# Optimization experiments

Hardware: AMD Instinct MI355X
Metric: run time of the kernel (lower is better)

Reference implementation:

```python
import jax, jax.numpy as jnp
import numpy as np

V, D, H, B, M, T, PAD = 32000, 512, 3, 32, 512, 4, 1


def setup_inputs() -> dict:
    key = jax.random.key(0)
    ks = jax.random.split(key, 10)
    def emb_tables(k):
        t = 0.1 * jax.random.normal(k, (H + 1, V, D), jnp.float32)
        return t.at[:, PAD, :].set(0.0)  # padding_idx rows are zero
    C_enc = emb_tables(ks[0])
    C_dec = emb_tables(ks[1])
    gru_w_ih = 0.1 * jax.random.normal(ks[2], (3 * D, D), jnp.float32)
    gru_w_hh = 0.1 * jax.random.normal(ks[3], (3 * D, D), jnp.float32)
    gru_b_ih = jnp.zeros((3 * D,), jnp.float32)
    gru_b_hh = jnp.zeros((3 * D,), jnp.float32)
    W1_w = 0.1 * jax.random.normal(ks[4], (V, 2 * D), jnp.float32)
    W1_b = jnp.zeros((V,), jnp.float32)
    story = jax.random.randint(ks[5], (B, M, T), 0, V, jnp.int32)
    enc_query = jax.random.randint(ks[6], (B,), 0, V, jnp.int32)
    return {"story": story, "enc_query": enc_query, "C_enc": C_enc,
            "C_dec": C_dec, "gru_w_ih": gru_w_ih, "gru_w_hh": gru_w_hh,
            "gru_b_ih": gru_b_ih, "gru_b_hh": gru_b_hh, "W1_w": W1_w,
            "W1_b": W1_b}


def _mem_embed(table, story):
    # table [V, D], story [B, M, T] -> sum-pooled memory [B, M, D]
    return jnp.sum(table[story], axis=2)


def _forward(C_enc, C_dec, gru_w_ih, gru_w_hh, gru_b_ih, gru_b_hh,
             W1_w, W1_b, story, enc_query):
    # ---- EncoderMemNN.forward (eval mode, no unk_mask dropout) ----
    u = jnp.zeros((story.shape[0], D), C_enc.dtype)
    for hop in range(H):
        m_A = _mem_embed(C_enc[hop], story)            # [B, M, D]
        prob = jax.nn.softmax(jnp.einsum('bmd,bd->bm', m_A, u), axis=1)
        m_C = _mem_embed(C_enc[hop + 1], story)        # [B, M, D]
        u = u + jnp.einsum('bmd,bm->bd', m_C, prob)
    enc_hidden = u                                     # decoder_hidden[0]

    # ---- DecoderrMemNN.ptrMemDecoder: single GRU step ----
    x = C_dec[0][enc_query]                            # [B, D]
    gi = x @ gru_w_ih.T + gru_b_ih                     # [B, 3D]
    gh = enc_hidden @ gru_w_hh.T + gru_b_hh            # [B, 3D]
    i_r, i_z, i_n = jnp.split(gi, 3, axis=1)
    h_r, h_z, h_n = jnp.split(gh, 3, axis=1)
    r = jax.nn.sigmoid(i_r + h_r)
    z = jax.nn.sigmoid(i_z + h_z)
    n = jnp.tanh(i_n + r * h_n)
    hidden = (1.0 - z) * n + z * enc_hidden            # new GRU hidden [B, D]

    # ---- DecoderrMemNN.load_memory: m_story[h] = sum-pooled C_dec[h] ----
    m_story = [_mem_embed(C_dec[h], story) for h in range(H + 1)]

    # ---- multi-hop pointer attention ----
    u0 = hidden
    uk = hidden
    p_vocab = None
    for hop in range(H):
        prob_lg = jnp.einsum('bmd,bd->bm', m_story[hop], uk)   # [B, M]
        prob = jax.nn.softmax(prob_lg, axis=1)
        o_k = jnp.einsum('bmd,bm->bd', m_story[hop + 1], prob)  # [B, D]
        if hop == 0:
            p_vocab = jnp.concatenate([u0, o_k], axis=1) @ W1_w.T + W1_b
        uk = uk + o_k
    p_ptr = prob_lg                                    # logits from last hop
    return p_ptr, p_vocab, hidden[None]                # hidden [1, B, D]


def reference(story, enc_query, C_enc, C_dec, gru_w_ih, gru_w_hh,
              gru_b_ih, gru_b_hh, W1_w, W1_b):
    return _forward(C_enc, C_dec, gru_w_ih, gru_w_hh, gru_b_ih, gru_b_hh,
                    W1_w, W1_b, story, enc_query)
```

## Files before the change

kernel.cpp:

```cpp
#include <hip/hip_runtime.h>
#include <math.h>

#define DD 512
#define MM 512
#define BB 32
#define TT 4
#define VV 32000

__global__ __launch_bounds__(256) void poolwsum_kernel(const float* __restrict__ table,
                                                       const int* __restrict__ story,
                                                       const float* __restrict__ s,
                                                       float* __restrict__ partial) {
  __shared__ float wrow[64];
  __shared__ int rows[64];
  __shared__ float red[16];
  __shared__ float4 comb[128];
  int b = blockIdx.x >> 5;
  int c = blockIdx.x & 31;
  int t = threadIdx.x;
  if (s) {
    float v0 = s[b * MM + t], v1 = s[b * MM + t + 256];
    float mx = fmaxf(v0, v1);
#pragma unroll
    for (int off = 32; off > 0; off >>= 1) mx = fmaxf(mx, __shfl_xor(mx, off));
    if ((t & 63) == 0) red[t >> 6] = mx;
    __syncthreads();
    mx = fmaxf(fmaxf(red[0], red[1]), fmaxf(red[2], red[3]));
    float e0 = expf(v0 - mx), e1 = expf(v1 - mx);
    float sm = e0 + e1;
#pragma unroll
    for (int off = 32; off > 0; off >>= 1) sm += __shfl_xor(sm, off);
    if ((t & 63) == 0) red[8 + (t >> 6)] = sm;
    __syncthreads();
    sm = red[8] + red[9] + red[10] + red[11];
    float inv = 1.0f / sm;
    if (t < 64) {
      rows[t] = story[((b << 9) + (c << 4)) * TT + t];
      wrow[t] = expf(s[b * MM + (c << 4) + (t >> 2)] - mx) * inv;
    }
  } else {
    if (t < 64) {
      rows[t] = story[((b << 9) + (c << 4)) * TT + t];
      wrow[t] = 1.0f / MM;
    }
  }
  __syncthreads();
  int half = t >> 7;
  int col = t & 127;
  float4 acc = make_float4(0.f, 0.f, 0.f, 0.f);
  for (int i = half; i < 64; i += 2) {
    float wm = wrow[i];
    float4 v = *((const float4*)(table + (size_t)rows[i] * DD) + col);
    acc.x += wm * v.x; acc.y += wm * v.y;
    acc.z += wm * v.z; acc.w += wm * v.w;
  }
  if (half) comb[col] = acc;
  __syncthreads();
  if (!half) {
    float4 o = comb[col];
    acc.x += o.x; acc.y += o.y; acc.z += o.z; acc.w += o.w;
    ((float4*)(partial + (size_t)blockIdx.x * DD))[col] = acc;
  }
}

__global__ void wsumB_kernel(const float* __restrict__ partial,
                             const float* __restrict__ prev,
                             float* __restrict__ uout) {
  int i = blockIdx.x * 256 + threadIdx.x;
  int b = i >> 9, d = i & 511;
  float acc = prev ? prev[i] : 0.f;
  const float* pp = partial + (size_t)b * 32 * DD + d;
#pragma unroll
  for (int c = 0; c < 32; ++c) acc += pp[c * DD];
  uout[i] = acc;
}

__global__ void wsumB2_kernel(const float* __restrict__ partial,
                              const float* __restrict__ hid,
                              float* __restrict__ uk, float* __restrict__ hc) {
  int i = blockIdx.x * 256 + threadIdx.x;
  int b = i >> 9, d = i & 511;
  float ov = 0.f;
  const float* pp = partial + (size_t)b * 32 * DD + d;
#pragma unroll
  for (int c = 0; c < 32; ++c) ov += pp[c * DD];
  float hv = hid[i];
  uk[i] = hv + ov;
  hc[b * 1024 + d] = hv;
  hc[b * 1024 + 512 + d] = ov;
}

__global__ __launch_bounds__(256) void pooldot_kernel(const float* __restrict__ table,
                                                      const int* __restrict__ story,
                                                      const float* __restrict__ u,
                                                      float* __restrict__ s) {
  int wave = (blockIdx.x << 2) + (threadIdx.x >> 6);
  int lane = threadIdx.x & 63;
  int b = wave >> 9;
  const int* st = story + wave * TT;
  size_t r0 = (size_t)st[0] * DD, r1 = (size_t)st[1] * DD;
  size_t r2 = (size_t)st[2] * DD, r3 = (size_t)st[3] * DD;
  const float4* t4 = (const float4*)table;
  const float4* ur = (const float4*)(u + (size_t)b * DD);
  float acc = 0.f;
#pragma unroll
  for (int h = 0; h < 2; ++h) {
    int c = (h << 6) + lane;
    float4 a = t4[(r0 >> 2) + c];
    float4 bb = t4[(r1 >> 2) + c];
    float4 cc = t4[(r2 >> 2) + c];
    float4 d = t4[(r3 >> 2) + c];
    float4 q = ur[c];
    acc += (a.x + bb.x + cc.x + d.x) * q.x;
    acc += (a.y + bb.y + cc.y + d.y) * q.y;
    acc += (a.z + bb.z + cc.z + d.z) * q.z;
    acc += (a.w + bb.w + cc.w + d.w) * q.w;
  }
#pragma unroll
  for (int off = 32; off > 0; off >>= 1) acc += __shfl_xor(acc, off);
  if (lane == 0) s[wave] = acc;
}

__global__ __launch_bounds__(256) void matvec_kernel(const float* __restrict__ W,
                                                     const float* __restrict__ bias,
                                                     const float* __restrict__ vin,
                                                     const int* __restrict__ q,
                                                     const float* __restrict__ table,
                                                     float* __restrict__ out) {
  int idx = (blockIdx.x << 2) + (threadIdx.x >> 6);
  int lane = threadIdx.x & 63;
  int b = idx / 1536;
  int j = idx - b * 1536;
  const float* xb = vin ? (vin + (size_t)b * DD) : (table + (size_t)q[b] * DD);
  const float4* Wr = (const float4*)(W + (size_t)j * DD);
  const float4* xr = (const float4*)xb;
  float acc = 0.f;
#pragma unroll
  for (int h = 0; h < 2; ++h) {
    int c = (h << 6) + lane;
    float4 a = Wr[c];
    float4 qv = xr[c];
    acc += a.x * qv.x + a.y * qv.y + a.z * qv.z + a.w * qv.w;
  }
#pragma unroll
  for (int off = 32; off > 0; off >>= 1) acc += __shfl_xor(acc, off);
  if (lane == 0) out[idx] = acc + bias[j];
}

__global__ void gate_kernel(const float* __restrict__ gi, const float* __restrict__ gh,
                            const float* __restrict__ u, float* __restrict__ hidden,
                            float* __restrict__ out_h) {
  int i = blockIdx.x * 256 + threadIdx.x;
  int b = i >> 9, d = i & 511;
  const float* gib = gi + b * 1536;
  const float* ghb = gh + b * 1536;
  float i_r = gib[d], i_z = gib[d + 512], i_n = gib[d + 1024];
  float h_r = ghb[d], h_z = ghb[d + 512], h_n = ghb[d + 1024];
  float r = 1.f / (1.f + expf(-(i_r + h_r)));
  float z = 1.f / (1.f + expf(-(i_z + h_z)));
  float n = tanhf(i_n + r * h_n);
  float h = (1.f - z) * n + z * u[i];
  hidden[i] = h;
  out_h[i] = h;
}

__global__ __launch_bounds__(256) void pvocab_kernel(const float* __restrict__ Hcat,
                                                     const float* __restrict__ W1,
                                                     float* __restrict__ partc) {
  __shared__ float As[32][36];
  __shared__ float Bs[32][68];
  int t = threadIdx.x;
  int vt = blockIdx.x >> 1;
  int kh = blockIdx.x & 1;
  int v0 = vt * 64;
  int kbase = kh << 9;
  int tb = t >> 5;
  int tv = t & 31;
  int br = t >> 2;
  int bk = (t & 3) << 3;
  const float* Wp = W1 + (size_t)(v0 + br) * 1024 + kbase + bk;
  int ab = t >> 3;
  int ak = (t & 7) << 2;
  const float* Ap = Hcat + (size_t)ab * 1024 + kbase + ak;

  float acc[4][2] = {{0.f, 0.f}, {0.f, 0.f}, {0.f, 0.f}, {0.f, 0.f}};

  float4 aReg = *(const float4*)(Ap);
  float4 wReg0 = *(const float4*)(Wp);
  float4 wReg1 = *(const float4*)(Wp + 4);

  for (int k0 = 0; k0 < 512; k0 += 32) {
    As[ak + 0][ab] = aReg.x; As[ak + 1][ab] = aReg.y;
    As[ak + 2][ab] = aReg.z; As[ak + 3][ab] = aReg.w;
    Bs[bk + 0][br] = wReg0.x; Bs[bk + 1][br] = wReg0.y;
    Bs[bk + 2][br] = wReg0.z; Bs[bk + 3][br] = wReg0.w;
    Bs[bk + 4][br] = wReg1.x; Bs[bk + 5][br] = wReg1.y;
    Bs[bk + 6][br] = wReg1.z; Bs[bk + 7][br] = wReg1.w;
    __syncthreads();
    if (k0 + 32 < 512) {
      aReg = *(const float4*)(Ap + k0 + 32);
      wReg0 = *(const float4*)(Wp + k0 + 32);
      wReg1 = *(const float4*)(Wp + k0 + 36);
    }
#pragma unroll
    for (int k = 0; k < 32; ++k) {
      float2 bv = *(const float2*)&Bs[k][tv * 2];
      float4 av = *(const float4*)&As[k][tb * 4];
      acc[0][0] += av.x * bv.x; acc[0][1] += av.x * bv.y;
      acc[1][0] += av.y * bv.x; acc[1][1] += av.y * bv.y;
      acc[2][0] += av.z * bv.x; acc[2][1] += av.z * bv.y;
      acc[3][0] += av.w * bv.x; acc[3][1] += av.w * bv.y;
    }
    __syncthreads();
  }
  int v = v0 + tv * 2;
  float* base = partc + (size_t)kh * 32 * VV;
#pragma unroll
  for (int i = 0; i < 4; ++i) {
    float2 r;
    r.x = acc[i][0];
    r.y = acc[i][1];
    *(float2*)(base + (size_t)(tb * 4 + i) * VV + v) = r;
  }
}

__global__ void pvreduce_kernel(const float* __restrict__ partc,
                                const float* __restrict__ W1b,
                                float* __restrict__ out) {
  int v = blockIdx.x * 256 + threadIdx.x;
  int b = blockIdx.y;
  size_t o = (size_t)b * VV + v;
  out[o] = partc[o] + partc[(size_t)32 * VV + o] + W1b[v];
}

extern "C" void kernel_launch(void* const* d_in, const int* in_sizes, int n_in,
                              void* d_out, int out_size, void* d_ws, size_t ws_size,
                              hipStream_t stream) {
  const int* story = (const int*)d_in[0];
  const int* q = (const int*)d_in[1];
  const float* C_enc = (const float*)d_in[2];
  const float* C_dec = (const float*)d_in[3];
  const float* W_ih = (const float*)d_in[4];
  const float* W_hh = (const float*)d_in[5];
  const float* b_ih = (const float*)d_in[6];
  const float* b_hh = (const float*)d_in[7];
  const float* W1 = (const float*)d_in[8];
  const float* W1b = (const float*)d_in[9];
  float* out = (float*)d_out;

  const size_t VD = (size_t)VV * DD;
  const float* C1 = C_enc + 1 * VD;
  const float* C2 = C_enc + 2 * VD;
  const float* C3 = C_enc + 3 * VD;
  const float* D0 = C_dec + 0 * VD;
  const float* D1 = C_dec + 1 * VD;
  const float* D2 = C_dec + 2 * VD;

  float* part = (float*)d_ws;
  float* partc = part + (size_t)BB * 32 * DD;
  float* u = partc + (size_t)2 * BB * VV;
  float* s = u + BB * DD;
  float* gi = s + BB * MM;
  float* gh = gi + BB * 3 * DD;
  float* hid = gh + BB * 3 * DD;
  float* uk = hid + BB * DD;
  float* hc = uk + BB * DD;

  float* p_ptr_out = out;
  float* p_vocab_out = out + BB * MM;
  float* hid_out = out + BB * MM + (size_t)BB * VV;

  dim3 blk(256);
  const int pwGrid = BB * 32;
  const int pdGrid = BB * MM / 4;
  const int mvGrid = BB * 3 * DD / 4;
  const int ewGrid = BB * DD / 256;

  poolwsum_kernel<<<pwGrid, blk, 0, stream>>>(C1, story, nullptr, part);
  wsumB_kernel<<<ewGrid, blk, 0, stream>>>(part, nullptr, u);
  pooldot_kernel<<<pdGrid, blk, 0, stream>>>(C1, story, u, s);
  poolwsum_kernel<<<pwGrid, blk, 0, stream>>>(C2, story, s, part);
  wsumB_kernel<<<ewGrid, blk, 0, stream>>>(part, u, u);
  pooldot_kernel<<<pdGrid, blk, 0, stream>>>(C2, story, u, s);
  poolwsum_kernel<<<pwGrid, blk, 0, stream>>>(C3, story, s, part);
  wsumB_kernel<<<ewGrid, blk, 0, stream>>>(part, u, u);

  matvec_kernel<<<mvGrid, blk, 0, stream>>>(W_ih, b_ih, nullptr, q, C_dec, gi);
  matvec_kernel<<<mvGrid, blk, 0, stream>>>(W_hh, b_hh, u, nullptr, nullptr, gh);
  gate_kernel<<<ewGrid, blk, 0, stream>>>(gi, gh, u, hid, hid_out);

  pooldot_kernel<<<pdGrid, blk, 0, stream>>>(D0, story, hid, s);
  poolwsum_kernel<<<pwGrid, blk, 0, stream>>>(D1, story, s, part);
  wsumB2_kernel<<<ewGrid, blk, 0, stream>>>(part, hid, uk, hc);
  pooldot_kernel<<<pdGrid, blk, 0, stream>>>(D1, story, uk, s);
  poolwsum_kernel<<<pwGrid, blk, 0, stream>>>(D2, story, s, part);
  wsumB_kernel<<<ewGrid, blk, 0, stream>>>(part, uk, uk);
  pooldot_kernel<<<pdGrid, blk, 0, stream>>>(D2, story, uk, p_ptr_out);

  pvocab_kernel<<<VV / 64 * 2, blk, 0, stream>>>(hc, W1, partc);
  pvreduce_kernel<<<dim3(125, 32), blk, 0, stream>>>(partc, W1b, p_vocab_out);
}
```

Measured before the change: 302.7 us.

## Replace gathered pooled dot with dense vocab GEMM plus index gather

Each pooled-memory dot product now scores every vocabulary row against u as a split-K GEMM (u times the table transposed). A light kernel then sums the precomputed scores at the four story indices per memory slot. The goal is to swap about 65K random 2KB row gathers per hop for one streaming read of the table. The cost is extra GEMM arithmetic and partial-score buffers written and re-read. The p_vocab GEMM also moves from 2-way to 4-way split-K, which doubles the block count but also the reduction traffic.

Result: slower. 373.5 us (+23.4%).

```diff
diff --git a/kernel.cpp b/kernel.cpp
--- a/kernel.cpp
+++ b/kernel.cpp
@@ -6,6 +6,7 @@
 #define BB 32
 #define TT 4
 #define VV 32000
+#define BV ((size_t)BB * VV)
 
 __global__ __launch_bounds__(256) void poolwsum_kernel(const float* __restrict__ table,
                                                        const int* __restrict__ story,
@@ -90,35 +91,79 @@
   hc[b * 1024 + 512 + d] = ov;
 }
 
-__global__ __launch_bounds__(256) void pooldot_kernel(const float* __restrict__ table,
-                                                      const int* __restrict__ story,
-                                                      const float* __restrict__ u,
-                                                      float* __restrict__ s) {
-  int wave = (blockIdx.x << 2) + (threadIdx.x >> 6);
-  int lane = threadIdx.x & 63;
-  int b = wave >> 9;
-  const int* st = story + wave * TT;
-  size_t r0 = (size_t)st[0] * DD, r1 = (size_t)st[1] * DD;
-  size_t r2 = (size_t)st[2] * DD, r3 = (size_t)st[3] * DD;
-  const float4* t4 = (const float4*)table;
-  const float4* ur = (const float4*)(u + (size_t)b * DD);
+__global__ __launch_bounds__(256) void dotV_kernel(const float* __restrict__ u,
+                                                   const float* __restrict__ C,
+                                                   float* __restrict__ part) {
+  __shared__ float As[32][36];
+  __shared__ float Bs[32][68];
+  int t = threadIdx.x;
+  int vt = blockIdx.x >> 2;
+  int kh = blockIdx.x & 3;
+  int v0 = vt * 64;
+  int kbase = kh << 7;
+  int tb = t >> 5;
+  int tv = t & 31;
+  int br = t >> 2;
+  int bk = (t & 3) << 3;
+  const float* Wp = C + (size_t)(v0 + br) * DD + kbase + bk;
+  int ab = t >> 3;
+  int ak = (t & 7) << 2;
+  const float* Ap = u + (size_t)ab * DD + kbase + ak;
+
+  float acc[4][2] = {{0.f, 0.f}, {0.f, 0.f}, {0.f, 0.f}, {0.f, 0.f}};
+
+  float4 aReg = *(const float4*)(Ap);
+  float4 wReg0 = *(const float4*)(Wp);
+  float4 wReg1 = *(const float4*)(Wp + 4);
+
+  for (int k0 = 0; k0 < 128; k0 += 32) {
+    As[ak + 0][ab] = aReg.x; As[ak + 1][ab] = aReg.y;
+    As[ak + 2][ab] = aReg.z; As[ak + 3][ab] = aReg.w;
+    Bs[bk + 0][br] = wReg0.x; Bs[bk + 1][br] = wReg0.y;
+    Bs[bk + 2][br] = wReg0.z; Bs[bk + 3][br] = wReg0.w;
+    Bs[bk + 4][br] = wReg1.x; Bs[bk + 5][br] = wReg1.y;
+    Bs[bk + 6][br] = wReg1.z; Bs[bk + 7][br] = wReg1.w;
+    __syncthreads();
+    if (k0 + 32 < 128) {
+      aReg = *(const float4*)(Ap + k0 + 32);
+      wReg0 = *(const float4*)(Wp + k0 + 32);
+      wReg1 = *(const float4*)(Wp + k0 + 36);
+    }
+#pragma unroll
+    for (int k = 0; k < 32; ++k) {
+      float2 bv = *(const float2*)&Bs[k][tv * 2];
+      float4 av = *(const float4*)&As[k][tb * 4];
+      acc[0][0] += av.x * bv.x; acc[0][1] += av.x * bv.y;
+      acc[1][0] += av.y * bv.x; acc[1][1] += av.y * bv.y;
+      acc[2][0] += av.z * bv.x; acc[2][1] += av.z * bv.y;
+      acc[3][0] += av.w * bv.x; acc[3][1] += av.w * bv.y;
+    }
+    __syncthreads();
+  }
+  int v = v0 + tv * 2;
+  float* base = part + (size_t)kh * BV;
+#pragma unroll
+  for (int i = 0; i < 4; ++i) {
+    float2 r;
+    r.x = acc[i][0];
+    r.y = acc[i][1];
+    *(float2*)(base + (size_t)(tb * 4 + i) * VV + v) = r;
+  }
+}
+
+__global__ void gatherS_kernel(const float* __restrict__ part,
+                               const int* __restrict__ story,
+                               float* __restrict__ outv) {
+  int i = blockIdx.x * 256 + threadIdx.x;
+  int b = i >> 9;
+  int4 ix = *(const int4*)(story + (size_t)i * 4);
   float acc = 0.f;
 #pragma unroll
-  for (int h = 0; h < 2; ++h) {
-    int c = (h << 6) + lane;
-    float4 a = t4[(r0 >> 2) + c];
-    float4 bb = t4[(r1 >> 2) + c];
-    float4 cc = t4[(r2 >> 2) + c];
-    float4 d = t4[(r3 >> 2) + c];
-    float4 q = ur[c];
-    acc += (a.x + bb.x + cc.x + d.x) * q.x;
-    acc += (a.y + bb.y + cc.y + d.y) * q.y;
-    acc += (a.z + bb.z + cc.z + d.z) * q.z;
-    acc += (a.w + bb.w + cc.w + d.w) * q.w;
-  }
-#pragma unroll
-  for (int off = 32; off > 0; off >>= 1) acc += __shfl_xor(acc, off);
-  if (lane == 0) s[wave] = acc;
+  for (int kh = 0; kh < 4; ++kh) {
+    const float* dv = part + (size_t)kh * BV + (size_t)b * VV;
+    acc += dv[ix.x] + dv[ix.y] + dv[ix.z] + dv[ix.w];
+  }
+  outv[i] = acc;
 }
 
 __global__ __launch_bounds__(256) void matvec_kernel(const float* __restrict__ W,
@@ -170,10 +215,10 @@
   __shared__ float As[32][36];
   __shared__ float Bs[32][68];
   int t = threadIdx.x;
-  int vt = blockIdx.x >> 1;
-  int kh = blockIdx.x & 1;
+  int vt = blockIdx.x >> 2;
+  int kh = blockIdx.x & 3;
   int v0 = vt * 64;
-  int kbase = kh << 9;
+  int kbase = kh << 8;
   int tb = t >> 5;
   int tv = t & 31;
   int br = t >> 2;
@@ -189,7 +234,7 @@
   float4 wReg0 = *(const float4*)(Wp);
   float4 wReg1 = *(const float4*)(Wp + 4);
 
-  for (int k0 = 0; k0 < 512; k0 += 32) {
+  for (int k0 = 0; k0 < 256; k0 += 32) {
     As[ak + 0][ab] = aReg.x; As[ak + 1][ab] = aReg.y;
     As[ak + 2][ab] = aReg.z; As[ak + 3][ab] = aReg.w;
     Bs[bk + 0][br] = wReg0.x; Bs[bk + 1][br] = wReg0.y;
@@ -197,7 +242,7 @@
     Bs[bk + 4][br] = wReg1.x; Bs[bk + 5][br] = wReg1.y;
     Bs[bk + 6][br] = wReg1.z; Bs[bk + 7][br] = wReg1.w;
     __syncthreads();
-    if (k0 + 32 < 512) {
+    if (k0 + 32 < 256) {
       aReg = *(const float4*)(Ap + k0 + 32);
       wReg0 = *(const float4*)(Wp + k0 + 32);
       wReg1 = *(const float4*)(Wp + k0 + 36);
@@ -214,7 +259,7 @@
     __syncthreads();
   }
   int v = v0 + tv * 2;
-  float* base = partc + (size_t)kh * 32 * VV;
+  float* base = partc + (size_t)kh * BV;
 #pragma unroll
   for (int i = 0; i < 4; ++i) {
     float2 r;
@@ -230,7 +275,7 @@
   int v = blockIdx.x * 256 + threadIdx.x;
   int b = blockIdx.y;
   size_t o = (size_t)b * VV + v;
-  out[o] = partc[o] + partc[(size_t)32 * VV + o] + W1b[v];
+  out[o] = partc[o] + partc[BV + o] + partc[2 * BV + o] + partc[3 * BV + o] + W1b[v];
 }
 
 extern "C" void kernel_launch(void* const* d_in, const int* in_sizes, int n_in,
@@ -258,7 +303,8 @@
 
   float* part = (float*)d_ws;
   float* partc = part + (size_t)BB * 32 * DD;
-  float* u = partc + (size_t)2 * BB * VV;
+  float* dvp = partc + 4 * BV;
+  float* u = dvp + 4 * BV;
   float* s = u + BB * DD;
   float* gi = s + BB * MM;
   float* gh = gi + BB * 3 * DD;
@@ -272,16 +318,18 @@
 
   dim3 blk(256);
   const int pwGrid = BB * 32;
-  const int pdGrid = BB * MM / 4;
+  const int dvGrid = VV / 64 * 4;
   const int mvGrid = BB * 3 * DD / 4;
   const int ewGrid = BB * DD / 256;
 
   poolwsum_kernel<<<pwGrid, blk, 0, stream>>>(C1, story, nullptr, part);
   wsumB_kernel<<<ewGrid, blk, 0, stream>>>(part, nullptr, u);
-  pooldot_kernel<<<pdGrid, blk, 0, stream>>>(C1, story, u, s);
+  dotV_kernel<<<dvGrid, blk, 0, stream>>>(u, C1, dvp);
+  gatherS_kernel<<<ewGrid, blk, 0, stream>>>(dvp, story, s);
   poolwsum_kernel<<<pwGrid, blk, 0, stream>>>(C2, story, s, part);
   wsumB_kernel<<<ewGrid, blk, 0, stream>>>(part, u, u);
-  pooldot_kernel<<<pdGrid, blk, 0, stream>>>(C2, story, u, s);
+  dotV_kernel<<<dvGrid, blk, 0, stream>>>(u, C2, dvp);
+  gatherS_kernel<<<ewGrid, blk, 0, stream>>>(dvp, story, s);
   poolwsum_kernel<<<pwGrid, blk, 0, stream>>>(C3, story, s, part);
   wsumB_kernel<<<ewGrid, blk, 0, stream>>>(part, u, u);
 
@@ -289,14 +337,17 @@
   matvec_kernel<<<mvGrid, blk, 0, stream>>>(W_hh, b_hh, u, nullptr, nullptr, gh);
   gate_kernel<<<ewGrid, blk, 0, stream>>>(gi, gh, u, hid, hid_out);
 
-  pooldot_kernel<<<pdGrid, blk, 0, stream>>>(D0, story, hid, s);
+  dotV_kernel<<<dvGrid, blk, 0, stream>>>(hid, D0, dvp);
+  gatherS_kernel<<<ewGrid, blk, 0, stream>>>(dvp, story, s);
   poolwsum_kernel<<<pwGrid, blk, 0, stream>>>(D1, story, s, part);
   wsumB2_kernel<<<ewGrid, blk, 0, stream>>>(part, hid, uk, hc);
-  pooldot_kernel<<<pdGrid, blk, 0, stream>>>(D1, story, uk, s);
+  dotV_kernel<<<dvGrid, blk, 0, stream>>>(uk, D1, dvp);
+  gatherS_kernel<<<ewGrid, blk, 0, stream>>>(dvp, story, s);
   poolwsum_kernel<<<pwGrid, blk, 0, stream>>>(D2, story, s, part);
   wsumB_kernel<<<ewGrid, blk, 0, stream>>>(part, uk, uk);
-  pooldot_kernel<<<pdGrid, blk, 0, stream>>>(D2, story, uk, p_ptr_out);
-
-  pvocab_kernel<<<VV / 64 * 2, blk, 0, stream>>>(hc, W1, partc);
+  dotV_kernel<<<dvGrid, blk, 0, stream>>>(uk, D2, dvp);
+  gatherS_kernel<<<ewGrid, blk, 0, stream>>>(dvp, story, p_ptr_out);
+
+  pvocab_kernel<<<dvGrid, blk, 0, stream>>>(hc, W1, partc);
   pvreduce_kernel<<<dim3(125, 32), blk, 0, stream>>>(partc, W1b, p_vocab_out);
 }
```

## Replace gathered memory pooling with scatter-to-vocab weights and dense table matvec

Applied to the files above, without the earlier changes.

The weighted sum over gathered embedding rows is reformulated in two steps. First, per-batch softmax weights are scattered into a dense [B, V] weight matrix using LDS atomics. Then every embedding table is streamed once, contiguously, as a dense batched product against those weights, and chunked partials are reduced afterwards. This swaps random 2KB row gathers, duplicated across batches and tokens, for one coalesced pass over the table. The cost is extra writes of the dense weight matrix and partials, a serial per-thread loop with only one step of prefetch, and just 250 blocks to cover the GPU.

Result: slower. 531.9 us (+75.7%).

```diff
diff --git a/kernel.cpp b/kernel.cpp
--- a/kernel.cpp
+++ b/kernel.cpp
@@ -6,18 +6,19 @@
 #define BB 32
 #define TT 4
 #define VV 32000
-
-__global__ __launch_bounds__(256) void poolwsum_kernel(const float* __restrict__ table,
+#define BV ((size_t)BB * VV)
+#define QN 8000
+#define NCHUNK 250
+
+__global__ __launch_bounds__(256) void wscatter_kernel(const float* __restrict__ s,
                                                        const int* __restrict__ story,
-                                                       const float* __restrict__ s,
-                                                       float* __restrict__ partial) {
-  __shared__ float wrow[64];
-  __shared__ int rows[64];
+                                                       float* __restrict__ accW) {
+  __shared__ float accl[QN];
+  __shared__ float wsm[MM];
   __shared__ float red[16];
-  __shared__ float4 comb[128];
-  int b = blockIdx.x >> 5;
-  int c = blockIdx.x & 31;
+  int q = blockIdx.x, b = blockIdx.y;
   int t = threadIdx.x;
+  int lo = q * QN, hi = lo + QN;
   if (s) {
     float v0 = s[b * MM + t], v1 = s[b * MM + t + 256];
     float mx = fmaxf(v0, v1);
@@ -34,60 +35,75 @@
     __syncthreads();
     sm = red[8] + red[9] + red[10] + red[11];
     float inv = 1.0f / sm;
-    if (t < 64) {
-      rows[t] = story[((b << 9) + (c << 4)) * TT + t];
-      wrow[t] = expf(s[b * MM + (c << 4) + (t >> 2)] - mx) * inv;
-    }
+    wsm[t] = e0 * inv;
+    wsm[t + 256] = e1 * inv;
   } else {
-    if (t < 64) {
-      rows[t] = story[((b << 9) + (c << 4)) * TT + t];
-      wrow[t] = 1.0f / MM;
-    }
-  }
+    wsm[t] = 1.0f / MM;
+    wsm[t + 256] = 1.0f / MM;
+  }
+  for (int i = t; i < QN; i += 256) accl[i] = 0.f;
   __syncthreads();
-  int half = t >> 7;
-  int col = t & 127;
-  float4 acc = make_float4(0.f, 0.f, 0.f, 0.f);
-  for (int i = half; i < 64; i += 2) {
-    float wm = wrow[i];
-    float4 v = *((const float4*)(table + (size_t)rows[i] * DD) + col);
-    acc.x += wm * v.x; acc.y += wm * v.y;
-    acc.z += wm * v.z; acc.w += wm * v.w;
-  }
-  if (half) comb[col] = acc;
+  const int* stb = story + (size_t)b * MM * TT;
+#pragma unroll
+  for (int j = 0; j < 8; ++j) {
+    int e = j * 256 + t;
+    int v = stb[e];
+    if (v >= lo && v < hi) atomicAdd(&accl[v - lo], wsm[e >> 2]);
+  }
   __syncthreads();
-  if (!half) {
-    float4 o = comb[col];
-    acc.x += o.x; acc.y += o.y; acc.z += o.z; acc.w += o.w;
-    ((float4*)(partial + (size_t)blockIdx.x * DD))[col] = acc;
-  }
-}
-
-__global__ void wsumB_kernel(const float* __restrict__ partial,
-                             const float* __restrict__ prev,
-                             float* __restrict__ uout) {
+  float* ob = accW + (size_t)b * VV + lo;
+  for (int i = t; i < QN; i += 256) ob[i] = accl[i];
+}
+
+__global__ __launch_bounds__(512) void wsumV_kernel(const float* __restrict__ table,
+                                                    const float* __restrict__ W,
+                                                    float* __restrict__ part) {
+  __shared__ float wsh[128 * 33];
+  int v0 = blockIdx.x << 7;
+  int t = threadIdx.x;
+#pragma unroll
+  for (int k = 0; k < 8; ++k) {
+    int idx = (k << 9) + t;
+    int b = idx >> 7, v = idx & 127;
+    wsh[v * 33 + b] = W[(size_t)b * VV + v0 + v];
+  }
+  __syncthreads();
+  float acc[32];
+#pragma unroll
+  for (int b = 0; b < 32; ++b) acc[b] = 0.f;
+  const float* tp = table + (size_t)v0 * DD + t;
+  float r = tp[0];
+  for (int v = 0; v < 128; ++v) {
+    float rn = (v < 127) ? tp[(size_t)(v + 1) * DD] : 0.f;
+#pragma unroll
+    for (int b = 0; b < 32; ++b) acc[b] += wsh[v * 33 + b] * r;
+    r = rn;
+  }
+  float* pp = part + (size_t)blockIdx.x * (32 * DD) + t;
+#pragma unroll
+  for (int b = 0; b < 32; ++b) pp[(size_t)b * DD] = acc[b];
+}
+
+__global__ void reduceV_kernel(const float* __restrict__ part,
+                               const float* __restrict__ prev,
+                               float* __restrict__ uout) {
+  int i = blockIdx.x * 256 + threadIdx.x;
+  float acc = 0.f;
+  for (int c = 0; c < NCHUNK; ++c) acc += part[(size_t)c * 16384 + i];
+  uout[i] = (prev ? prev[i] : 0.f) + acc;
+}
+
+__global__ void reduceV2_kernel(const float* __restrict__ part,
+                                const float* __restrict__ hid,
+                                float* __restrict__ uk, float* __restrict__ hc) {
   int i = blockIdx.x * 256 + threadIdx.x;
   int b = i >> 9, d = i & 511;
-  float acc = prev ? prev[i] : 0.f;
-  const float* pp = partial + (size_t)b * 32 * DD + d;
-#pragma unroll
-  for (int c = 0; c < 32; ++c) acc += pp[c * DD];
-  uout[i] = acc;
-}
-
-__global__ void wsumB2_kernel(const float* __restrict__ partial,
-                              const float* __restrict__ hid,
-                              float* __restrict__ uk, float* __restrict__ hc) {
-  int i = blockIdx.x * 256 + threadIdx.x;
-  int b = i >> 9, d = i & 511;
-  float ov = 0.f;
-  const float* pp = partial + (size_t)b * 32 * DD + d;
-#pragma unroll
-  for (int c = 0; c < 32; ++c) ov += pp[c * DD];
+  float o = 0.f;
+  for (int c = 0; c < NCHUNK; ++c) o += part[(size_t)c * 16384 + i];
   float hv = hid[i];
-  uk[i] = hv + ov;
+  uk[i] = hv + o;
   hc[b * 1024 + d] = hv;
-  hc[b * 1024 + 512 + d] = ov;
+  hc[b * 1024 + 512 + d] = o;
 }
 
 __global__ __launch_bounds__(256) void pooldot_kernel(const float* __restrict__ table,
@@ -214,7 +230,7 @@
     __syncthreads();
   }
   int v = v0 + tv * 2;
-  float* base = partc + (size_t)kh * 32 * VV;
+  float* base = partc + (size_t)kh * BV;
 #pragma unroll
   for (int i = 0; i < 4; ++i) {
     float2 r;
@@ -230,7 +246,7 @@
   int v = blockIdx.x * 256 + threadIdx.x;
   int b = blockIdx.y;
   size_t o = (size_t)b * VV + v;
-  out[o] = partc[o] + partc[(size_t)32 * VV + o] + W1b[v];
+  out[o] = partc[o] + partc[BV + o] + W1b[v];
 }
 
 extern "C" void kernel_launch(void* const* d_in, const int* in_sizes, int n_in,
@@ -256,9 +272,10 @@
   const float* D1 = C_dec + 1 * VD;
   const float* D2 = C_dec + 2 * VD;
 
-  float* part = (float*)d_ws;
-  float* partc = part + (size_t)BB * 32 * DD;
-  float* u = partc + (size_t)2 * BB * VV;
+  float* accW = (float*)d_ws;
+  float* part = accW + BV;
+  float* partc = part + (size_t)NCHUNK * 32 * DD;
+  float* u = partc + 2 * BV;
   float* s = u + BB * DD;
   float* gi = s + BB * MM;
   float* gh = gi + BB * 3 * DD;
@@ -271,30 +288,35 @@
   float* hid_out = out + BB * MM + (size_t)BB * VV;
 
   dim3 blk(256);
-  const int pwGrid = BB * 32;
+  const dim3 wsGrid(4, BB);
   const int pdGrid = BB * MM / 4;
   const int mvGrid = BB * 3 * DD / 4;
   const int ewGrid = BB * DD / 256;
 
-  poolwsum_kernel<<<pwGrid, blk, 0, stream>>>(C1, story, nullptr, part);
-  wsumB_kernel<<<ewGrid, blk, 0, stream>>>(part, nullptr, u);
+  wscatter_kernel<<<wsGrid, blk, 0, stream>>>(nullptr, story, accW);
+  wsumV_kernel<<<NCHUNK, dim3(512), 0, stream>>>(C1, accW, part);
+  reduceV_kernel<<<ewGrid, blk, 0, stream>>>(part, nullptr, u);
   pooldot_kernel<<<pdGrid, blk, 0, stream>>>(C1, story, u, s);
-  poolwsum_kernel<<<pwGrid, blk, 0, stream>>>(C2, story, s, part);
-  wsumB_kernel<<<ewGrid, blk, 0, stream>>>(part, u, u);
+  wscatter_kernel<<<wsGrid, blk, 0, stream>>>(s, story, accW);
+  wsumV_kernel<<<NCHUNK, dim3(512), 0, stream>>>(C2, accW, part);
+  reduceV_kernel<<<ewGrid, blk, 0, stream>>>(part, u, u);
   pooldot_kernel<<<pdGrid, blk, 0, stream>>>(C2, story, u, s);
-  poolwsum_kernel<<<pwGrid, blk, 0, stream>>>(C3, story, s, part);
-  wsumB_kernel<<<ewGrid, blk, 0, stream>>>(part, u, u);
+  wscatter_kernel<<<wsGrid, blk, 0, stream>>>(s, story, accW);
+  wsumV_kernel<<<NCHUNK, dim3(512), 0, stream>>>(C3, accW, part);
+  reduceV_kernel<<<ewGrid, blk, 0, stream>>>(part, u, u);
 
   matvec_kernel<<<mvGrid, blk, 0, stream>>>(W_ih, b_ih, nullptr, q, C_dec, gi);
   matvec_kernel<<<mvGrid, blk, 0, stream>>>(W_hh, b_hh, u, nullptr, nullptr, gh);
   gate_kernel<<<ewGrid, blk, 0, stream>>>(gi, gh, u, hid, hid_out);
 
   pooldot_kernel<<<pdGrid, blk, 0, stream>>>(D0, story, hid, s);
-  poolwsum_kernel<<<pwGrid, blk, 0, stream>>>(D1, story, s, part);
-  wsumB2_kernel<<<ewGrid, blk, 0, stream>>>(part, hid, uk, hc);
+  wscatter_kernel<<<wsGrid, blk, 0, stream>>>(s, story, accW);
+  wsumV_kernel<<<NCHUNK, dim3(512), 0, stream>>>(D1, accW, part);
+  reduceV2_kernel<<<ewGrid, blk, 0, stream>>>(part, hid, uk, hc);
   pooldot_kernel<<<pdGrid, blk, 0, stream>>>(D1, story, uk, s);
-  poolwsum_kernel<<<pwGrid, blk, 0, stream>>>(D2, story, s, part);
-  wsumB_kernel<<<ewGrid, blk, 0, stream>>>(part, uk, uk);
+  wscatter_kernel<<<wsGrid, blk, 0, stream>>>(s, story, accW);
+  wsumV_kernel<<<NCHUNK, dim3(512), 0, stream>>>(D2, accW, part);
+  reduceV_kernel<<<ewGrid, blk, 0, stream>>>(part, uk, uk);
   pooldot_kernel<<<pdGrid, blk, 0, stream>>>(D2, story, uk, p_ptr_out);
 
   pvocab_kernel<<<VV / 64 * 2, blk, 0, stream>>>(hc, W1, partc);
```

## Materialize pooled memory once and reuse it for subsequent dot-product passes

Applied to the files above, without the earlier changes.

The weighted-sum kernel now writes the sum-pooled memory rows P[B,M,D] while it gathers them. The following attention-logit pass reads these contiguous pooled rows through a new Pdot kernel instead of re-gathering and summing 4 random embedding rows per slot. This replaces scattered gathers from the large tables with streaming reads of a 32 MB buffer, at the cost of an extra 32 MB write in each pooling pass that produces P. The workspace grows by B*M*D floats.

Measured after the change: 268.4 us. 11.3% less time.

```diff
diff --git a/kernel.cpp b/kernel.cpp
--- a/kernel.cpp
+++ b/kernel.cpp
@@ -6,12 +6,14 @@
 #define BB 32
 #define TT 4
 #define VV 32000
-
-__global__ __launch_bounds__(256) void poolwsum_kernel(const float* __restrict__ table,
-                                                       const int* __restrict__ story,
-                                                       const float* __restrict__ s,
-                                                       float* __restrict__ partial) {
-  __shared__ float wrow[64];
+#define BV ((size_t)BB * VV)
+
+__global__ __launch_bounds__(256) void poolwsumP_kernel(const float* __restrict__ table,
+                                                        const int* __restrict__ story,
+                                                        const float* __restrict__ s,
+                                                        float* __restrict__ P,
+                                                        float* __restrict__ partial) {
+  __shared__ float wrow[16];
   __shared__ int rows[64];
   __shared__ float red[16];
   __shared__ float4 comb[128];
@@ -34,32 +36,62 @@
     __syncthreads();
     sm = red[8] + red[9] + red[10] + red[11];
     float inv = 1.0f / sm;
-    if (t < 64) {
-      rows[t] = story[((b << 9) + (c << 4)) * TT + t];
-      wrow[t] = expf(s[b * MM + (c << 4) + (t >> 2)] - mx) * inv;
-    }
+    if (t < 16) wrow[t] = expf(s[b * MM + (c << 4) + t] - mx) * inv;
   } else {
-    if (t < 64) {
-      rows[t] = story[((b << 9) + (c << 4)) * TT + t];
-      wrow[t] = 1.0f / MM;
-    }
-  }
+    if (t < 16) wrow[t] = 1.0f / MM;
+  }
+  if (t < 64) rows[t] = story[((b << 9) + (c << 4)) * TT + t];
   __syncthreads();
-  int half = t >> 7;
+  int h = t >> 7;
   int col = t & 127;
   float4 acc = make_float4(0.f, 0.f, 0.f, 0.f);
-  for (int i = half; i < 64; i += 2) {
-    float wm = wrow[i];
-    float4 v = *((const float4*)(table + (size_t)rows[i] * DD) + col);
-    acc.x += wm * v.x; acc.y += wm * v.y;
-    acc.z += wm * v.z; acc.w += wm * v.w;
-  }
-  if (half) comb[col] = acc;
+#pragma unroll
+  for (int i = 0; i < 8; ++i) {
+    int lm = (i << 1) + h;
+    const float4* r0 = (const float4*)(table + (size_t)rows[lm * 4 + 0] * DD);
+    const float4* r1 = (const float4*)(table + (size_t)rows[lm * 4 + 1] * DD);
+    const float4* r2 = (const float4*)(table + (size_t)rows[lm * 4 + 2] * DD);
+    const float4* r3 = (const float4*)(table + (size_t)rows[lm * 4 + 3] * DD);
+    float4 a = r0[col], bb = r1[col], cc = r2[col], d = r3[col];
+    float4 pooled;
+    pooled.x = a.x + bb.x + cc.x + d.x;
+    pooled.y = a.y + bb.y + cc.y + d.y;
+    pooled.z = a.z + bb.z + cc.z + d.z;
+    pooled.w = a.w + bb.w + cc.w + d.w;
+    if (P) ((float4*)(P + ((size_t)(b << 9) + (c << 4) + lm) * DD))[col] = pooled;
+    float wm = wrow[lm];
+    acc.x += wm * pooled.x; acc.y += wm * pooled.y;
+    acc.z += wm * pooled.z; acc.w += wm * pooled.w;
+  }
+  if (h) comb[col] = acc;
   __syncthreads();
-  if (!half) {
+  if (!h) {
     float4 o = comb[col];
     acc.x += o.x; acc.y += o.y; acc.z += o.z; acc.w += o.w;
     ((float4*)(partial + (size_t)blockIdx.x * DD))[col] = acc;
+  }
+}
+
+__global__ __launch_bounds__(256) void Pdot_kernel(const float* __restrict__ P,
+                                                   const float* __restrict__ u,
+                                                   float* __restrict__ s) {
+  int b = blockIdx.x >> 5;
+  int c = blockIdx.x & 31;
+  int w = threadIdx.x >> 6;
+  int lane = threadIdx.x & 63;
+  const float4* ur = (const float4*)(u + (size_t)b * DD);
+  float4 u0 = ur[lane], u1 = ur[lane + 64];
+  const float4* Pb = (const float4*)(P + ((size_t)(b << 9) + (c << 4)) * DD);
+#pragma unroll
+  for (int j = 0; j < 4; ++j) {
+    int m = (w << 2) + j;
+    const float4* pr = Pb + (size_t)m * 128;
+    float4 a = pr[lane], bb = pr[lane + 64];
+    float acc = a.x * u0.x + a.y * u0.y + a.z * u0.z + a.w * u0.w
+              + bb.x * u1.x + bb.y * u1.y + bb.z * u1.z + bb.w * u1.w;
+#pragma unroll
+    for (int off = 32; off > 0; off >>= 1) acc += __shfl_xor(acc, off);
+    if (lane == 0) s[(b << 9) + (c << 4) + m] = acc;
   }
 }
 
@@ -214,7 +246,7 @@
     __syncthreads();
   }
   int v = v0 + tv * 2;
-  float* base = partc + (size_t)kh * 32 * VV;
+  float* base = partc + (size_t)kh * BV;
 #pragma unroll
   for (int i = 0; i < 4; ++i) {
     float2 r;
@@ -230,7 +262,7 @@
   int v = blockIdx.x * 256 + threadIdx.x;
   int b = blockIdx.y;
   size_t o = (size_t)b * VV + v;
-  out[o] = partc[o] + partc[(size_t)32 * VV + o] + W1b[v];
+  out[o] = partc[o] + partc[BV + o] + W1b[v];
 }
 
 extern "C" void kernel_launch(void* const* d_in, const int* in_sizes, int n_in,
@@ -256,9 +288,10 @@
   const float* D1 = C_dec + 1 * VD;
   const float* D2 = C_dec + 2 * VD;
 
-  float* part = (float*)d_ws;
+  float* P = (float*)d_ws;
+  float* part = P + (size_t)BB * MM * DD;
   float* partc = part + (size_t)BB * 32 * DD;
-  float* u = partc + (size_t)2 * BB * VV;
+  float* u = partc + 2 * BV;
   float* s = u + BB * DD;
   float* gi = s + BB * MM;
   float* gh = gi + BB * 3 * DD;
@@ -273,16 +306,17 @@
   dim3 blk(256);
   const int pwGrid = BB * 32;
   const int pdGrid = BB * MM / 4;
+  const int PdGrid = BB * 32;
   const int mvGrid = BB * 3 * DD / 4;
   const int ewGrid = BB * DD / 256;
 
-  poolwsum_kernel<<<pwGrid, blk, 0, stream>>>(C1, story, nullptr, part);
+  poolwsumP_kernel<<<pwGrid, blk, 0, stream>>>(C1, story, nullptr, P, part);
   wsumB_kernel<<<ewGrid, blk, 0, stream>>>(part, nullptr, u);
-  pooldot_kernel<<<pdGrid, blk, 0, stream>>>(C1, story, u, s);
-  poolwsum_kernel<<<pwGrid, blk, 0, stream>>>(C2, story, s, part);
+  Pdot_kernel<<<PdGrid, blk, 0, stream>>>(P, u, s);
+  poolwsumP_kernel<<<pwGrid, blk, 0, stream>>>(C2, story, s, P, part);
   wsumB_kernel<<<ewGrid, blk, 0, stream>>>(part, u, u);
-  pooldot_kernel<<<pdGrid, blk, 0, stream>>>(C2, story, u, s);
-  poolwsum_kernel<<<pwGrid, blk, 0, stream>>>(C3, story, s, part);
+  Pdot_kernel<<<PdGrid, blk, 0, stream>>>(P, u, s);
+  poolwsumP_kernel<<<pwGrid, blk, 0, stream>>>(C3, story, s, nullptr, part);
   wsumB_kernel<<<ewGrid, blk, 0, stream>>>(part, u, u);
 
   matvec_kernel<<<mvGrid, blk, 0, stream>>>(W_ih, b_ih, nullptr, q, C_dec, gi);
@@ -290,12 +324,12 @@
   gate_kernel<<<ewGrid, blk, 0, stream>>>(gi, gh, u, hid, hid_out);
 
   pooldot_kernel<<<pdGrid, blk, 0, stream>>>(D0, story, hid, s);
-  poolwsum_kernel<<<pwGrid, blk, 0, stream>>>(D1, story, s, part);
+  poolwsumP_kernel<<<pwGrid, blk, 0, stream>>>(D1, story, s, P, part);
   wsumB2_kernel<<<ewGrid, blk, 0, stream>>>(part, hid, uk, hc);
-  pooldot_kernel<<<pdGrid, blk, 0, stream>>>(D1, story, uk, s);
-  poolwsum_kernel<<<pwGrid, blk, 0, stream>>>(D2, story, s, part);
+  Pdot_kernel<<<PdGrid, blk, 0, stream>>>(P, uk, s);
+  poolwsumP_kernel<<<pwGrid, blk, 0, stream>>>(D2, story, s, P, part);
   wsumB_kernel<<<ewGrid, blk, 0, stream>>>(part, uk, uk);
-  pooldot_kernel<<<pdGrid, blk, 0, stream>>>(D2, story, uk, p_ptr_out);
+  Pdot_kernel<<<PdGrid, blk, 0, stream>>>(P, uk, p_ptr_out);
 
   pvocab_kernel<<<VV / 64 * 2, blk, 0, stream>>>(hc, W1, partc);
   pvreduce_kernel<<<dim3(125, 32), blk, 0, stream>>>(partc, W1b, p_vocab_out);
```
